# Kernel tuning notes

Measured on AMD Instinct MI355X. Metric: run time of the kernel, lower is better.

The kernel has to match this reference:

```python
import jax, jax.numpy as jnp
import numpy as np

GROUPSIZE = 128
# 6 possible 2:4 sparsity patterns (choose 2 nonzeros out of each group of 4 rows)
_PATTERNS = jnp.array([
    [1, 1, 0, 0], [1, 0, 1, 0], [1, 0, 0, 1],
    [0, 1, 1, 0], [0, 1, 0, 1], [0, 0, 1, 1],
], dtype=jnp.float32)


def setup_inputs() -> dict:
    key = jax.random.key(0)
    k1, k2, k3, k4 = jax.random.split(key, 4)
    M, K, N = 4096, 4096, 8192
    x = jax.random.normal(k1, (M, K), dtype=jnp.float16)
    # int4 codes in [0, 15] (stored unpacked; bit-packing is layout-only)
    qweight = jax.random.randint(k2, (K, N), 0, 16, dtype=jnp.int32)
    # 2:4 pattern index per group of 4 consecutive K rows
    meta = jax.random.randint(k3, (K // 4, N), 0, 6, dtype=jnp.int32)
    # positive group scales, typical quantization magnitude
    scale = (jax.random.uniform(k4, (K // GROUPSIZE, N), dtype=jnp.float32) * 0.02 + 0.005).astype(jnp.float16)
    return {"x": x, "qweight": qweweight_fix(qweight), "meta": meta, "scale": scale}


def qweweight_fix(q):
    return q  # identity; kept for clarity


def _dequant(qweight, meta, scale):
    """Dequantize int4 2:4-sparse weights with group scales -> dense fp32 [K, N]."""
    K, N = qweight.shape
    mask = _PATTERNS[meta]                      # [K//4, N, 4]
    mask = jnp.transpose(mask, (0, 2, 1)).reshape(K, N)  # [K, N]
    s = jnp.repeat(scale.astype(jnp.float32), GROUPSIZE, axis=0)  # [K, N]
    # symmetric int4: zero-point = 8 (maxq+1)//2
    return (qweight.astype(jnp.float32) - 8.0) * mask * s


def reference(x, qweight, meta, scale):
    W = _dequant(qweight, meta, scale)          # [K, N] fp32
    out = x.astype(jnp.float32) @ W             # fp32 accumulation, as in the kernel
    return out.astype(x.dtype)                  # [M, N] fp16
```

## Files before the change

### kernel.cpp

```cpp
#include <hip/hip_runtime.h>
#include <cmath>


typedef __attribute__((ext_vector_type(8))) short bf16x8;
typedef __attribute__((ext_vector_type(4))) float f32x4;

__device__ inline unsigned short f2bf(float f) {
    union { float f; unsigned u; } v; v.f = f;
    unsigned r = (v.u + 0x7FFFu + ((v.u >> 16) & 1u)) >> 16;
    return (unsigned short)r;
}

__global__ __launch_bounds__(256) void convert_x(
    const float* __restrict__ x, unsigned short* __restrict__ xb, long long total)
{
    const long long base = ((long long)blockIdx.x * 256 + threadIdx.x) * 8;
    if (base + 8 > total) return;
    const float4 a = *reinterpret_cast<const float4*>(x + base);
    const float4 b = *reinterpret_cast<const float4*>(x + base + 4);
    uint4 o;
    o.x = (unsigned)f2bf(a.x) | ((unsigned)f2bf(a.y) << 16);
    o.y = (unsigned)f2bf(a.z) | ((unsigned)f2bf(a.w) << 16);
    o.z = (unsigned)f2bf(b.x) | ((unsigned)f2bf(b.y) << 16);
    o.w = (unsigned)f2bf(b.z) | ((unsigned)f2bf(b.w) << 16);
    *reinterpret_cast<uint4*>(xb + base) = o;
}

__global__ __launch_bounds__(256) void dequant_wt(
    const int* __restrict__ q, const int* __restrict__ meta,
    const float* __restrict__ scale,
    unsigned short* __restrict__ wt,
    int K, int N, int nbase)
{
    __shared__ __align__(16) unsigned short lds[64 * 68];
    const int t  = threadIdx.x;
    const int n  = t & 63;
    const int kc = t >> 6;
    const int k0 = blockIdx.x * 64;
    const int nl0 = blockIdx.y * 64;
    const int ng = nbase + nl0 + n;
    const int g = k0 >> 7;
    const float sc = scale[(size_t)g * N + ng];
    const unsigned lut = 0xCA6953u;

    #pragma unroll
    for (int p = 0; p < 4; ++p) {
        const int kl = p * 16 + kc * 4;
        const int kg = k0 + kl;
        const int mv = meta[(size_t)(kg >> 2) * N + ng];
        const unsigned pat = (lut >> (mv * 4)) & 0xFu;
        unsigned short w[4];
        #pragma unroll
        for (int j = 0; j < 4; ++j) {
            const int qv = q[(size_t)(kg + j) * N + ng];
            const float wf = ((pat >> j) & 1u) ? (float)(qv - 8) * sc : 0.0f;
            w[j] = f2bf(wf);
        }
        uint2 pk;
        pk.x = (unsigned)w[0] | ((unsigned)w[1] << 16);
        pk.y = (unsigned)w[2] | ((unsigned)w[3] << 16);
        *reinterpret_cast<uint2*>(&lds[n * 68 + kl]) = pk;
    }
    __syncthreads();
    #pragma unroll
    for (int p = 0; p < 2; ++p) {
        const int idx = p * 256 + t;
        const int nr  = idx >> 3;
        const int ch  = idx & 7;
        const uint2 lo = *reinterpret_cast<const uint2*>(&lds[nr * 68 + ch * 8]);
        const uint2 hi = *reinterpret_cast<const uint2*>(&lds[nr * 68 + ch * 8 + 4]);
        uint4 vv; vv.x = lo.x; vv.y = lo.y; vv.z = hi.x; vv.w = hi.y;
        *reinterpret_cast<uint4*>(&wt[(size_t)(nl0 + nr) * K + k0 + ch * 8]) = vv;
    }
}

#define BAR() do { asm volatile("" ::: "memory"); \
                   __builtin_amdgcn_s_barrier(); \
                   asm volatile("" ::: "memory"); } while (0)

#define GLDS(g, s) __builtin_amdgcn_global_load_lds( \
    (const __attribute__((address_space(1))) void*)(g), \
    (__attribute__((address_space(3))) void*)(s), 16, 0, 0)

#define MFMA(d, x, y) d = __builtin_amdgcn_mfma_f32_16x16x32_bf16(x, y, d, 0, 0, 0)

__global__ __launch_bounds__(512, 2) void gemm256(
    const unsigned short* __restrict__ A,
    const unsigned short* __restrict__ Bt,
    float* __restrict__ C,
    int M, int N, int K, int nbase)
{
    __shared__ __align__(16) unsigned short As[32768];
    __shared__ __align__(16) unsigned short Bs[32768];

    const int t    = threadIdx.x;
    const int w    = t >> 6;
    const int lane = t & 63;
    const int wm   = w >> 2;
    const int wn   = w & 3;
    const int l16  = lane & 15;
    const int quad = lane >> 4;

    const int gx = gridDim.x, gy = gridDim.y;
    int bid = blockIdx.y * gx + blockIdx.x;
    const int nwg = gx * gy;
    int m0, n0;
    if ((nwg & 7) == 0 && (gy & 1) == 0 && (gx & 3) == 0) {
        const int xcd = bid & 7;
        const int idx = bid >> 3;
        const int cpr = gx >> 2;
        const int lr  = idx / cpr;
        const int lc  = idx - lr * cpr;
        m0 = ((xcd >> 2) * (gy >> 1) + lr) * 256;
        n0 = ((xcd & 3) * cpr + lc) * 256;
    } else {
        int b2 = bid;
        if (nwg >= 8) {
            const int q8 = nwg >> 3, r8 = nwg & 7;
            const int xcd = bid & 7, off = bid >> 3;
            b2 = (xcd < r8 ? xcd * (q8 + 1) : r8 * (q8 + 1) + (xcd - r8) * q8) + off;
        }
        n0 = (b2 % gx) * 256;
        m0 = (b2 / gx) * 256;
    }

    const int    csrc = ((lane & 7) ^ ((lane >> 3) & 7)) * 8;
    const size_t aB = (size_t)(m0 + w * 8 + (lane >> 3)) * K + csrc;
    const size_t bB = (size_t)(n0 + w * 8 + (lane >> 3)) * K + csrc;
    const size_t J  = (size_t)64 * K;
    const size_t H  = (size_t)128 * K;
    const int sdst  = w * 512;

    const int sw0 = ((quad ^ (lane & 7)) * 8);
    const int sw1 = (((4 + quad) ^ (lane & 7)) * 8);
    const int aR  = wm * 8192 + l16 * 64;
    const int bR  = (wn >> 1) * 8192 + ((wn & 1) * 64 + l16) * 64;

    int kA = 0, kB = 0;

#define STAGE_A(buf, h) do { \
    GLDS(A + aB + (size_t)(h) * H + kA, &As[(buf)*16384 + (h)*8192 + sdst]); \
    GLDS(A + aB + (size_t)(h) * H + J + kA, &As[(buf)*16384 + (h)*8192 + 4096 + sdst]); \
  } while (0)
#define STAGE_B(buf, h) do { \
    GLDS(Bt + bB + (size_t)(h) * H + kB, &Bs[(buf)*16384 + (h)*8192 + sdst]); \
    GLDS(Bt + bB + (size_t)(h) * H + J + kB, &Bs[(buf)*16384 + (h)*8192 + 4096 + sdst]); \
  } while (0)

    f32x4 acc[8][4];
    #pragma unroll
    for (int i = 0; i < 8; ++i)
        #pragma unroll
        for (int j = 0; j < 4; ++j)
            acc[i][j] = (f32x4){0.f, 0.f, 0.f, 0.f};

    STAGE_B(0, 0); STAGE_B(0, 1); kB += 64;
    STAGE_A(0, 0); STAGE_A(0, 1); kA += 64;
    STAGE_B(1, 0); STAGE_B(1, 1); kB += 64;
    asm volatile("s_waitcnt vmcnt(4)" ::: "memory");
    BAR();

    bf16x8 a[4][2], bA_[2][2], bB_[2][2];

    #pragma unroll
    for (int j = 0; j < 2; ++j) {
        bA_[j][0] = *(const bf16x8*)&Bs[bR + j * 1024 + sw0];
        bA_[j][1] = *(const bf16x8*)&Bs[bR + j * 1024 + sw1];
    }

#define PHASES(buf, obuf, bcur, bnxt) do { \
   \
  _Pragma("unroll") for (int i = 0; i < 4; ++i) { \
    a[i][0] = *(const bf16x8*)&As[(buf)*16384 + aR + i*1024 + sw0]; \
    a[i][1] = *(const bf16x8*)&As[(buf)*16384 + aR + i*1024 + sw1]; } \
  STAGE_A(obuf, 0); STAGE_A(obuf, 1); kA += 64; if (kA >= K) kA = 0; \
  BAR(); \
  asm volatile("s_waitcnt lgkmcnt(0)" ::: "memory"); \
  __builtin_amdgcn_s_setprio(1); \
  _Pragma("unroll") for (int i = 0; i < 4; ++i) \
    _Pragma("unroll") for (int j = 0; j < 2; ++j) { \
      MFMA(acc[i][j], a[i][0], bcur[j][0]); MFMA(acc[i][j], a[i][1], bcur[j][1]); } \
  __builtin_amdgcn_s_setprio(0); \
  BAR(); \
   \
  _Pragma("unroll") for (int j = 0; j < 2; ++j) { \
    bnxt[j][0] = *(const bf16x8*)&Bs[(buf)*16384 + bR + (2+j)*1024 + sw0]; \
    bnxt[j][1] = *(const bf16x8*)&Bs[(buf)*16384 + bR + (2+j)*1024 + sw1]; } \
  BAR(); \
  asm volatile("s_waitcnt lgkmcnt(0)" ::: "memory"); \
  __builtin_amdgcn_s_setprio(1); \
  _Pragma("unroll") for (int i = 0; i < 4; ++i) \
    _Pragma("unroll") for (int j = 0; j < 2; ++j) { \
      MFMA(acc[i][2+j], a[i][0], bnxt[j][0]); MFMA(acc[i][2+j], a[i][1], bnxt[j][1]); } \
  __builtin_amdgcn_s_setprio(0); \
  BAR(); \
   \
  _Pragma("unroll") for (int i = 0; i < 4; ++i) { \
    a[i][0] = *(const bf16x8*)&As[(buf)*16384 + aR + (4+i)*1024 + sw0]; \
    a[i][1] = *(const bf16x8*)&As[(buf)*16384 + aR + (4+i)*1024 + sw1]; } \
  STAGE_B(buf, 0); \
  BAR(); \
  asm volatile("s_waitcnt lgkmcnt(0)" ::: "memory"); \
  __builtin_amdgcn_s_setprio(1); \
  _Pragma("unroll") for (int i = 0; i < 4; ++i) \
    _Pragma("unroll") for (int j = 0; j < 2; ++j) { \
      MFMA(acc[4+i][2+j], a[i][0], bnxt[j][0]); MFMA(acc[4+i][2+j], a[i][1], bnxt[j][1]); } \
  __builtin_amdgcn_s_setprio(0); \
  BAR(); \
   \
   \
  asm volatile("s_waitcnt vmcnt(6)" ::: "memory"); \
  _Pragma("unroll") for (int j = 0; j < 2; ++j) { \
    bnxt[j][0] = *(const bf16x8*)&Bs[(obuf)*16384 + bR + j*1024 + sw0]; \
    bnxt[j][1] = *(const bf16x8*)&Bs[(obuf)*16384 + bR + j*1024 + sw1]; } \
  STAGE_B(buf, 1); kB += 64; if (kB >= K) kB = 0; \
  BAR(); \
  asm volatile("s_waitcnt lgkmcnt(0)" ::: "memory"); \
  __builtin_amdgcn_s_setprio(1); \
  _Pragma("unroll") for (int i = 0; i < 4; ++i) \
    _Pragma("unroll") for (int j = 0; j < 2; ++j) { \
      MFMA(acc[4+i][j], a[i][0], bcur[j][0]); MFMA(acc[4+i][j], a[i][1], bcur[j][1]); } \
  __builtin_amdgcn_s_setprio(0); \
  asm volatile("s_waitcnt vmcnt(4)" ::: "memory"); \
  BAR(); \
} while (0)

    const int NIT = K >> 7;
    for (int it = 0; it < NIT; ++it) {
        PHASES(0, 1, bA_, bB_);
        PHASES(1, 0, bB_, bA_);
    }

    asm volatile("s_waitcnt vmcnt(0)" ::: "memory");

    const int mBase = m0 + wm * 128;
    const int nBase = nbase + n0 + wn * 64;
    #pragma unroll
    for (int i = 0; i < 8; ++i) {
        const int mrow = mBase + i * 16 + quad * 4;
        #pragma unroll
        for (int j = 0; j < 4; ++j) {
            const int ncol = nBase + j * 16 + l16;
            #pragma unroll
            for (int r = 0; r < 4; ++r)
                C[(size_t)(mrow + r) * N + ncol] = acc[i][j][r];
        }
    }
#undef STAGE_A
#undef STAGE_B
#undef PHASES
}

extern "C" void kernel_launch(void* const* d_in, const int* in_sizes, int n_in,
                              void* d_out, int out_size, void* d_ws, size_t ws_size,
                              hipStream_t stream)
{
    const float* x     = (const float*)d_in[0];
    const int*   q     = (const int*)d_in[1];
    const int*   meta  = (const int*)d_in[2];
    const float* scale = (const float*)d_in[3];
    float*       out   = (float*)d_out;

    const double s0 = (double)in_sizes[0];
    const double s1 = (double)in_sizes[1];
    const int K = (int)llround(sqrt(s0 * s1 / (double)out_size));
    const int M = in_sizes[0] / K;
    const int N = in_sizes[1] / K;

    unsigned short* xb = (unsigned short*)d_ws;
    const size_t xb_bytes = (size_t)M * (size_t)K * 2;
    unsigned short* wt = (unsigned short*)((char*)d_ws + xb_bytes);
    const size_t wt_avail = ws_size > xb_bytes ? ws_size - xb_bytes : 0;

    const long long total = (long long)M * K;
    convert_x<<<dim3((unsigned)((total / 8 + 255) / 256)), dim3(256), 0, stream>>>(
        x, xb, total);

    long long maxrows = (long long)(wt_avail / ((size_t)K * 2));
    int NC = (int)((maxrows / 256) * 256);
    if (NC > N) NC = N;
    if (NC < 256) NC = 256;

    for (int nbase = 0; nbase < N; nbase += NC) {
        const int nc = (N - nbase) < NC ? (N - nbase) : NC;
        dim3 g1(K / 64, nc / 64);
        dequant_wt<<<g1, dim3(256), 0, stream>>>(q, meta, scale, wt, K, N, nbase);
        dim3 g2(nc / 256, M / 256);
        gemm256<<<g2, dim3(512), 0, stream>>>(xb, wt, out, M, N, K, nbase);
    }
}
```

Baseline: 560.9 us.

## Fuse int4 2:4 weight dequantization into the GEMM B-tile staging

Removes the separate dequant kernel and the bf16 weight workspace. The GEMM now loads int32 codes, 2:4 pattern indices and group scales per tile directly into registers, dequantizes them, and writes swizzled bf16 into shared memory. The B-tile loads are rescheduled between the MFMA phases. This avoids writing and re-reading a dense bf16 weight matrix, but each row-block re-reads the 4-byte int32 codes, and the per-tile arithmetic, register pressure and vmcnt(0) waits grow inside the main loop.

Measured after the change: 831.4 us. +48.2%, slower.

```diff
diff --git a/kernel.cpp b/kernel.cpp
--- a/kernel.cpp
+++ b/kernel.cpp
@@ -4,6 +4,7 @@
 
 typedef __attribute__((ext_vector_type(8))) short bf16x8;
 typedef __attribute__((ext_vector_type(4))) float f32x4;
+typedef __attribute__((ext_vector_type(4))) unsigned int u32x4;
 
 __device__ inline unsigned short f2bf(float f) {
     union { float f; unsigned u; } v; v.f = f;
@@ -18,60 +19,12 @@
     if (base + 8 > total) return;
     const float4 a = *reinterpret_cast<const float4*>(x + base);
     const float4 b = *reinterpret_cast<const float4*>(x + base + 4);
-    uint4 o;
+    u32x4 o;
     o.x = (unsigned)f2bf(a.x) | ((unsigned)f2bf(a.y) << 16);
     o.y = (unsigned)f2bf(a.z) | ((unsigned)f2bf(a.w) << 16);
     o.z = (unsigned)f2bf(b.x) | ((unsigned)f2bf(b.y) << 16);
     o.w = (unsigned)f2bf(b.z) | ((unsigned)f2bf(b.w) << 16);
-    *reinterpret_cast<uint4*>(xb + base) = o;
-}
-
-__global__ __launch_bounds__(256) void dequant_wt(
-    const int* __restrict__ q, const int* __restrict__ meta,
-    const float* __restrict__ scale,
-    unsigned short* __restrict__ wt,
-    int K, int N, int nbase)
-{
-    __shared__ __align__(16) unsigned short lds[64 * 68];
-    const int t  = threadIdx.x;
-    const int n  = t & 63;
-    const int kc = t >> 6;
-    const int k0 = blockIdx.x * 64;
-    const int nl0 = blockIdx.y * 64;
-    const int ng = nbase + nl0 + n;
-    const int g = k0 >> 7;
-    const float sc = scale[(size_t)g * N + ng];
-    const unsigned lut = 0xCA6953u;
-
-    #pragma unroll
-    for (int p = 0; p < 4; ++p) {
-        const int kl = p * 16 + kc * 4;
-        const int kg = k0 + kl;
-        const int mv = meta[(size_t)(kg >> 2) * N + ng];
-        const unsigned pat = (lut >> (mv * 4)) & 0xFu;
-        unsigned short w[4];
-        #pragma unroll
-        for (int j = 0; j < 4; ++j) {
-            const int qv = q[(size_t)(kg + j) * N + ng];
-            const float wf = ((pat >> j) & 1u) ? (float)(qv - 8) * sc : 0.0f;
-            w[j] = f2bf(wf);
-        }
-        uint2 pk;
-        pk.x = (unsigned)w[0] | ((unsigned)w[1] << 16);
-        pk.y = (unsigned)w[2] | ((unsigned)w[3] << 16);
-        *reinterpret_cast<uint2*>(&lds[n * 68 + kl]) = pk;
-    }
-    __syncthreads();
-    #pragma unroll
-    for (int p = 0; p < 2; ++p) {
-        const int idx = p * 256 + t;
-        const int nr  = idx >> 3;
-        const int ch  = idx & 7;
-        const uint2 lo = *reinterpret_cast<const uint2*>(&lds[nr * 68 + ch * 8]);
-        const uint2 hi = *reinterpret_cast<const uint2*>(&lds[nr * 68 + ch * 8 + 4]);
-        uint4 vv; vv.x = lo.x; vv.y = lo.y; vv.z = hi.x; vv.w = hi.y;
-        *reinterpret_cast<uint4*>(&wt[(size_t)(nl0 + nr) * K + k0 + ch * 8]) = vv;
-    }
+    *reinterpret_cast<u32x4*>(xb + base) = o;
 }
 
 #define BAR() do { asm volatile("" ::: "memory"); \
@@ -86,9 +39,11 @@
 
 __global__ __launch_bounds__(512, 2) void gemm256(
     const unsigned short* __restrict__ A,
-    const unsigned short* __restrict__ Bt,
+    const int* __restrict__ Q,
+    const int* __restrict__ Meta,
+    const float* __restrict__ Scale,
     float* __restrict__ C,
-    int M, int N, int K, int nbase)
+    int M, int N, int K)
 {
     __shared__ __align__(16) unsigned short As[32768];
     __shared__ __align__(16) unsigned short Bs[32768];
@@ -126,10 +81,19 @@
 
     const int    csrc = ((lane & 7) ^ ((lane >> 3) & 7)) * 8;
     const size_t aB = (size_t)(m0 + w * 8 + (lane >> 3)) * K + csrc;
-    const size_t bB = (size_t)(n0 + w * 8 + (lane >> 3)) * K + csrc;
     const size_t J  = (size_t)64 * K;
     const size_t H  = (size_t)128 * K;
     const int sdst  = w * 512;
+
+    const int brow = w * 32 + (lane & 31);
+    const int cb   = (lane >> 5) * 4;
+    const int bn   = n0 + brow;
+    const int* __restrict__ qcol = Q + bn;
+    const int* __restrict__ mcol = Meta + bn;
+    const float* __restrict__ scol = Scale + bn;
+    const int bwr  = (brow >> 7) * 8192 + (brow & 127) * 64;
+    const int r7   = brow & 7;
+    const unsigned lut = 0xCA6953u;
 
     const int sw0 = ((quad ^ (lane & 7)) * 8);
     const int sw1 = (((4 + quad) ^ (lane & 7)) * 8);
@@ -142,9 +106,42 @@
     GLDS(A + aB + (size_t)(h) * H + kA, &As[(buf)*16384 + (h)*8192 + sdst]); \
     GLDS(A + aB + (size_t)(h) * H + J + kA, &As[(buf)*16384 + (h)*8192 + 4096 + sdst]); \
   } while (0)
-#define STAGE_B(buf, h) do { \
-    GLDS(Bt + bB + (size_t)(h) * H + kB, &Bs[(buf)*16384 + (h)*8192 + sdst]); \
-    GLDS(Bt + bB + (size_t)(h) * H + J + kB, &Bs[(buf)*16384 + (h)*8192 + 4096 + sdst]); \
+
+    int   qreg[4][8];
+    int   mreg[4][2];
+    float screg;
+
+#define BSTAGE_LOAD() do { \
+    screg = scol[(size_t)(kB >> 7) * N]; \
+    _Pragma("unroll") for (int g = 0; g < 4; ++g) { \
+      const int kk = kB + (cb + g) * 8; \
+      mreg[g][0] = mcol[(size_t)((kk >> 2) + 0) * N]; \
+      mreg[g][1] = mcol[(size_t)((kk >> 2) + 1) * N]; \
+      _Pragma("unroll") for (int j = 0; j < 8; ++j) \
+        qreg[g][j] = qcol[(size_t)(kk + j) * N]; \
+    } \
+  } while (0)
+
+#define BSTAGE_WRITE(buf) do { \
+    _Pragma("unroll") for (int g = 0; g < 4; ++g) { \
+      const int slot = (cb + g) ^ r7; \
+      u32x4 pk; \
+      _Pragma("unroll") for (int pp = 0; pp < 4; ++pp) { \
+        unsigned short wv0, wv1; \
+        { const int j = pp * 2; \
+          const int mv = mreg[g][j >> 2]; \
+          const float wf = ((lut >> (mv * 4 + (j & 3))) & 1u) \
+              ? (float)(qreg[g][j] - 8) * screg : 0.0f; \
+          wv0 = f2bf(wf); } \
+        { const int j = pp * 2 + 1; \
+          const int mv = mreg[g][j >> 2]; \
+          const float wf = ((lut >> (mv * 4 + (j & 3))) & 1u) \
+              ? (float)(qreg[g][j] - 8) * screg : 0.0f; \
+          wv1 = f2bf(wf); } \
+        pk[pp] = (unsigned)wv0 | ((unsigned)wv1 << 16); \
+      } \
+      *reinterpret_cast<u32x4*>(&Bs[(buf) * 16384 + bwr + slot * 8]) = pk; \
+    } \
   } while (0)
 
     f32x4 acc[8][4];
@@ -154,10 +151,16 @@
         for (int j = 0; j < 4; ++j)
             acc[i][j] = (f32x4){0.f, 0.f, 0.f, 0.f};
 
-    STAGE_B(0, 0); STAGE_B(0, 1); kB += 64;
+    BSTAGE_LOAD();
     STAGE_A(0, 0); STAGE_A(0, 1); kA += 64;
-    STAGE_B(1, 0); STAGE_B(1, 1); kB += 64;
     asm volatile("s_waitcnt vmcnt(4)" ::: "memory");
+    BSTAGE_WRITE(0);
+    kB += 64;
+    BSTAGE_LOAD();
+    asm volatile("s_waitcnt vmcnt(0)" ::: "memory");
+    BSTAGE_WRITE(1);
+    kB += 64;
+    asm volatile("s_waitcnt lgkmcnt(0)" ::: "memory");
     BAR();
 
     bf16x8 a[4][2], bA_[2][2], bB_[2][2];
@@ -173,7 +176,7 @@
   _Pragma("unroll") for (int i = 0; i < 4; ++i) { \
     a[i][0] = *(const bf16x8*)&As[(buf)*16384 + aR + i*1024 + sw0]; \
     a[i][1] = *(const bf16x8*)&As[(buf)*16384 + aR + i*1024 + sw1]; } \
-  STAGE_A(obuf, 0); STAGE_A(obuf, 1); kA += 64; if (kA >= K) kA = 0; \
+  STAGE_A(obuf, 0); \
   BAR(); \
   asm volatile("s_waitcnt lgkmcnt(0)" ::: "memory"); \
   __builtin_amdgcn_s_setprio(1); \
@@ -186,6 +189,8 @@
   _Pragma("unroll") for (int j = 0; j < 2; ++j) { \
     bnxt[j][0] = *(const bf16x8*)&Bs[(buf)*16384 + bR + (2+j)*1024 + sw0]; \
     bnxt[j][1] = *(const bf16x8*)&Bs[(buf)*16384 + bR + (2+j)*1024 + sw1]; } \
+  STAGE_A(obuf, 1); kA += 64; if (kA >= K) kA = 0; \
+  BSTAGE_LOAD(); kB += 64; if (kB >= K) kB = 0; \
   BAR(); \
   asm volatile("s_waitcnt lgkmcnt(0)" ::: "memory"); \
   __builtin_amdgcn_s_setprio(1); \
@@ -198,7 +203,6 @@
   _Pragma("unroll") for (int i = 0; i < 4; ++i) { \
     a[i][0] = *(const bf16x8*)&As[(buf)*16384 + aR + (4+i)*1024 + sw0]; \
     a[i][1] = *(const bf16x8*)&As[(buf)*16384 + aR + (4+i)*1024 + sw1]; } \
-  STAGE_B(buf, 0); \
   BAR(); \
   asm volatile("s_waitcnt lgkmcnt(0)" ::: "memory"); \
   __builtin_amdgcn_s_setprio(1); \
@@ -209,19 +213,18 @@
   BAR(); \
    \
    \
-  asm volatile("s_waitcnt vmcnt(6)" ::: "memory"); \
+   \
+  __builtin_amdgcn_s_setprio(1); \
+  _Pragma("unroll") for (int i = 0; i < 4; ++i) \
+    _Pragma("unroll") for (int j = 0; j < 2; ++j) { \
+      MFMA(acc[4+i][j], a[i][0], bcur[j][0]); MFMA(acc[4+i][j], a[i][1], bcur[j][1]); } \
+  __builtin_amdgcn_s_setprio(0); \
+  asm volatile("s_waitcnt vmcnt(0)" ::: "memory"); \
+  BSTAGE_WRITE(buf); \
   _Pragma("unroll") for (int j = 0; j < 2; ++j) { \
     bnxt[j][0] = *(const bf16x8*)&Bs[(obuf)*16384 + bR + j*1024 + sw0]; \
     bnxt[j][1] = *(const bf16x8*)&Bs[(obuf)*16384 + bR + j*1024 + sw1]; } \
-  STAGE_B(buf, 1); kB += 64; if (kB >= K) kB = 0; \
-  BAR(); \
-  asm volatile("s_waitcnt lgkmcnt(0)" ::: "memory"); \
-  __builtin_amdgcn_s_setprio(1); \
-  _Pragma("unroll") for (int i = 0; i < 4; ++i) \
-    _Pragma("unroll") for (int j = 0; j < 2; ++j) { \
-      MFMA(acc[4+i][j], a[i][0], bcur[j][0]); MFMA(acc[4+i][j], a[i][1], bcur[j][1]); } \
-  __builtin_amdgcn_s_setprio(0); \
-  asm volatile("s_waitcnt vmcnt(4)" ::: "memory"); \
+  asm volatile("s_waitcnt lgkmcnt(0)" ::: "memory"); \
   BAR(); \
 } while (0)
 
@@ -234,7 +237,7 @@
     asm volatile("s_waitcnt vmcnt(0)" ::: "memory");
 
     const int mBase = m0 + wm * 128;
-    const int nBase = nbase + n0 + wn * 64;
+    const int nBase = n0 + wn * 64;
     #pragma unroll
     for (int i = 0; i < 8; ++i) {
         const int mrow = mBase + i * 16 + quad * 4;
@@ -247,7 +250,8 @@
         }
     }
 #undef STAGE_A
-#undef STAGE_B
+#undef BSTAGE_LOAD
+#undef BSTAGE_WRITE
 #undef PHASES
 }
 
@@ -268,24 +272,11 @@
     const int N = in_sizes[1] / K;
 
     unsigned short* xb = (unsigned short*)d_ws;
-    const size_t xb_bytes = (size_t)M * (size_t)K * 2;
-    unsigned short* wt = (unsigned short*)((char*)d_ws + xb_bytes);
-    const size_t wt_avail = ws_size > xb_bytes ? ws_size - xb_bytes : 0;
-
     const long long total = (long long)M * K;
+
     convert_x<<<dim3((unsigned)((total / 8 + 255) / 256)), dim3(256), 0, stream>>>(
         x, xb, total);
 
-    long long maxrows = (long long)(wt_avail / ((size_t)K * 2));
-    int NC = (int)((maxrows / 256) * 256);
-    if (NC > N) NC = N;
-    if (NC < 256) NC = 256;
-
-    for (int nbase = 0; nbase < N; nbase += NC) {
-        const int nc = (N - nbase) < NC ? (N - nbase) : NC;
-        dim3 g1(K / 64, nc / 64);
-        dequant_wt<<<g1, dim3(256), 0, stream>>>(q, meta, scale, wt, K, N, nbase);
-        dim3 g2(nc / 256, M / 256);
-        gemm256<<<g2, dim3(512), 0, stream>>>(xb, wt, out, M, N, K, nbase);
-    }
-}
+    dim3 g2(N / 256, M / 256);
+    gemm256<<<g2, dim3(512), 0, stream>>>(xb, q, meta, scale, out, M, N, K);
+}
```
